# Kernel optimization log

Measured on AMD Instinct MI355X. Metric: run time of the kernel, lower is better.

## Reference

```python
import jax, jax.numpy as jnp
import numpy as np

T = 36  # num_frames


def box_cxcywh_to_xyxy(b):
    cx, cy, w, h = jnp.split(b, 4, axis=-1)
    return jnp.concatenate([cx - 0.5 * w, cy - 0.5 * h, cx + 0.5 * w, cy + 0.5 * h], axis=-1)


def multi_iou(b1, b2):
    # b1: [Q,1,T,4], b2: [1,N,T,4], xyxy -> iou [Q,N,T]
    lt = jnp.maximum(b1[..., :2], b2[..., :2])
    rb = jnp.minimum(b1[..., 2:], b2[..., 2:])
    wh = jnp.clip(rb - lt, 0.0)
    inter = wh[..., 0] * wh[..., 1]
    a1 = (b1[..., 2] - b1[..., 0]) * (b1[..., 3] - b1[..., 1])
    a2 = (b2[..., 2] - b2[..., 0]) * (b2[..., 3] - b2[..., 1])
    union = a1 + a2 - inter
    return inter / union


def setup_inputs() -> dict:
    key = jax.random.key(0)
    k1, k2, k3, k4, k5, k6 = jax.random.split(key, 6)
    Q, N, C = 2048, 128, 42
    return {
        "pred_logits": jax.random.normal(k1, (T * Q, C), dtype=jnp.float32),
        "pred_boxes": jax.random.uniform(k2, (T * Q, 4), dtype=jnp.float32),
        "tgt_labels": jax.random.randint(k3, (N * T,), 0, C - 1),
        "tgt_boxes": jax.random.uniform(k4, (N * T, 4), dtype=jnp.float32),
        "tgt_valid": jax.random.randint(k5, (N * T,), 0, 2, dtype=jnp.int32),
        "tgt_original_valid": jax.random.randint(k6, (N * T,), 0, 2, dtype=jnp.int32),
    }


def reference(pred_logits, pred_boxes, tgt_labels, tgt_boxes, tgt_valid, tgt_original_valid):
    # Cost-matrix computation of SoftMaxHungarianMatcher (cost_class=cost_bbox=cost_giou=1,
    # use_giou=False, use_l1_distance_sum=False). The scipy linear_sum_assignment step is
    # CPU-serial / non-tensor and excluded; output is the [Q,N] cost fed to it.
    C = pred_logits.shape[-1]
    Q = pred_logits.shape[0] // T
    N = tgt_labels.shape[0] // T
    num_classes = C - 1  # background index

    probs = jax.nn.softmax(pred_logits, axis=-1).reshape(T, Q, C).transpose(1, 0, 2)  # [Q,T,C]
    boxes = pred_boxes.reshape(T, Q, 4).transpose(1, 0, 2)                            # [Q,T,4]
    tboxes = tgt_boxes.reshape(N, T, 4)
    valid = tgt_valid.reshape(N, T).astype(probs.dtype)                               # [N,T]
    ovalid = tgt_original_valid.reshape(N, T)
    ids = jnp.where(ovalid == 0, num_classes, tgt_labels.reshape(N, T))               # [N,T]

    denom = valid.sum(-1)  # [N] (per-instance count of valid frames)

    # class cost: -mean_t p(q, t, ids[n,t]) over valid frames
    gathered = probs[:, jnp.arange(T)[None, :], ids]                                  # [Q,N,T]
    class_cost = -(gathered * valid).sum(-1) / denom                                  # [Q,N]

    # bbox L1 cost: mean over (valid frames, 4 coords)
    l1 = jnp.abs(boxes[:, None] - tboxes[None]).mean(-1)                              # [Q,N,T]
    bbox_cost = (l1 * valid).sum(-1) / denom                                          # [Q,N]

    # IoU cost: -mean_t iou over valid frames
    iou = multi_iou(box_cxcywh_to_xyxy(boxes)[:, None], box_cxcywh_to_xyxy(tboxes)[None])
    iou_cost = -(iou * valid).sum(-1) / denom                                         # [Q,N]

    return class_cost + bbox_cost + iou_cost
```

## Files before the change

kernel.cpp:

```cpp
#include <hip/hip_runtime.h>
#include <hip/hip_bf16.h>


constexpr int T = 36;
constexpr int Q = 2048;
constexpr int C = 42;
constexpr int N = 128;
constexpr int QB = 8;

__global__ __launch_bounds__(1024) void fused_kernel(
    const float* __restrict__ logits, const float* __restrict__ pboxes,
    const int* __restrict__ labels, const float* __restrict__ tboxes,
    const int* __restrict__ valid, const int* __restrict__ ovalid,
    float* __restrict__ out) {
  __shared__ float s_p[T * QB * C];
  __shared__ unsigned int s_idv[N * 9];
  __shared__ float s_out[QB * N];

  const int tid = threadIdx.x;
  const int q0 = blockIdx.x * QB;

  for (int i = tid; i < N * 9; i += 1024) {
    int n = i / 9;
    int t4 = (i - n * 9) * 4;
    unsigned int w = 0;
#pragma unroll
    for (int k = 0; k < 4; ++k) {
      int g = n * T + t4 + k;
      unsigned int id =
          (ovalid[g] == 0) ? (unsigned)(C - 1) : (unsigned)labels[g];
      w |= (id | (valid[g] ? 64u : 0u)) << (8 * k);
    }
    s_idv[i] = w;
  }

  for (int i = tid; i < T * 84; i += 1024) {
    int t = i / 84;
    int idx = i - t * 84;
    float4 v = ((const float4*)(logits + ((size_t)t * Q + q0) * C))[idx];
    float4 e;
    e.x = __expf(v.x);
    e.y = __expf(v.y);
    e.z = __expf(v.z);
    e.w = __expf(v.w);
    ((float4*)s_p)[t * 84 + idx] = e;
  }
  __syncthreads();

  if (tid < T * QB * 2) {
    const int r = tid >> 1;
    const int half = tid & 1;
    float* rowp = s_p + r * C + half * 21;
    float e[21];
    float s = 0.f;
#pragma unroll
    for (int k = 0; k < 21; ++k) {
      e[k] = rowp[k];
      s += e[k];
    }
    s += __shfl_xor(s, 1);
    float rs = __builtin_amdgcn_rcpf(s);
#pragma unroll
    for (int k = 0; k < 21; ++k) rowp[k] = e[k] * rs;
  }
  __syncthreads();

  const int qL = tid & 7;
  const int n = tid >> 3;
  const int q = q0 + qL;

  float acc = 0.f, sumv = 0.f;
  const unsigned int* idvp = s_idv + n * 9;
  const float* prow = s_p + qL * C;

  for (int tw = 0; tw < 9; ++tw) {
    unsigned int w = idvp[tw];
#pragma unroll
    for (int k = 0; k < 4; ++k) {
      const int t = tw * 4 + k;
      unsigned int b = (w >> (8 * k)) & 0xFFu;
      float vf = (float)(b >> 6);
      int id = (int)(b & 63u);
      float p = prow[(t * QB) * C + id];
      float4 pb = ((const float4*)pboxes)[t * Q + q];
      float4 tb = ((const float4*)tboxes)[n * T + t];

      float px1 = fmaf(-0.5f, pb.z, pb.x), py1 = fmaf(-0.5f, pb.w, pb.y);
      float px2 = fmaf(0.5f, pb.z, pb.x), py2 = fmaf(0.5f, pb.w, pb.y);
      float tx1 = fmaf(-0.5f, tb.z, tb.x), ty1 = fmaf(-0.5f, tb.w, tb.y);
      float tx2 = fmaf(0.5f, tb.z, tb.x), ty2 = fmaf(0.5f, tb.w, tb.y);

      float s4 = fabsf(pb.x - tb.x) + fabsf(pb.y - tb.y) +
                 fabsf(pb.z - tb.z) + fabsf(pb.w - tb.w);
      float iw = fmaxf(fminf(px2, tx2) - fmaxf(px1, tx1), 0.f);
      float ih = fmaxf(fminf(py2, ty2) - fmaxf(py1, ty1), 0.f);
      float inter = iw * ih;
      float uni = fmaf(tb.z, tb.w, pb.z * pb.w) - inter;
      float iou = inter * __builtin_amdgcn_rcpf(uni);
      float term = fmaf(0.25f, s4, -p) - iou;
      acc = fmaf(vf, term, acc);
      sumv += vf;
    }
  }

  s_out[qL * N + n] = acc * __builtin_amdgcn_rcpf(sumv);
  __syncthreads();

  if (tid < 256) {
    int qr = tid >> 5;
    int nf = tid & 31;
    float4 v = ((const float4*)s_out)[qr * 32 + nf];
    ((float4*)out)[(size_t)(q0 + qr) * (N / 4) + nf] = v;
  }
}

extern "C" void kernel_launch(void* const* d_in, const int* in_sizes, int n_in,
                              void* d_out, int out_size, void* d_ws, size_t ws_size,
                              hipStream_t stream) {
  const float* logits = (const float*)d_in[0];
  const float* pboxes = (const float*)d_in[1];
  const int* labels = (const int*)d_in[2];
  const float* tboxes = (const float*)d_in[3];
  const int* valid = (const int*)d_in[4];
  const int* ovalid = (const int*)d_in[5];
  float* out = (float*)d_out;

  fused_kernel<<<dim3(Q / QB), 1024, 0, stream>>>(logits, pboxes, labels,
                                                  tboxes, valid, ovalid, out);
}
```

Measured before the change: 84.55 us.

## Halve queries per block, split frames across thread halves, defer softmax normalization

New measurement: 84.65 us. Within noise of the previous version (+0.1%).

```diff
diff --git a/kernel.cpp b/kernel.cpp
--- a/kernel.cpp
+++ b/kernel.cpp
@@ -6,15 +6,18 @@
 constexpr int Q = 2048;
 constexpr int C = 42;
 constexpr int N = 128;
-constexpr int QB = 8;
+constexpr int QB = 4;
 
-__global__ __launch_bounds__(1024) void fused_kernel(
+__global__ __launch_bounds__(1024, 8) void fused_kernel(
     const float* __restrict__ logits, const float* __restrict__ pboxes,
     const int* __restrict__ labels, const float* __restrict__ tboxes,
     const int* __restrict__ valid, const int* __restrict__ ovalid,
     float* __restrict__ out) {
   __shared__ float s_p[T * QB * C];
   __shared__ unsigned int s_idv[N * 9];
+  __shared__ float s_rs[T * QB];
+  __shared__ float s_rden[N];
+  __shared__ float s_red[512];
   __shared__ float s_out[QB * N];
 
   const int tid = threadIdx.x;
@@ -34,56 +37,62 @@
     s_idv[i] = w;
   }
 
-  for (int i = tid; i < T * 84; i += 1024) {
-    int t = i / 84;
-    int idx = i - t * 84;
+  for (int i = tid; i < T * 42; i += 1024) {
+    int t = i / 42;
+    int idx = i - t * 42;
     float4 v = ((const float4*)(logits + ((size_t)t * Q + q0) * C))[idx];
     float4 e;
     e.x = __expf(v.x);
     e.y = __expf(v.y);
     e.z = __expf(v.z);
     e.w = __expf(v.w);
-    ((float4*)s_p)[t * 84 + idx] = e;
+    ((float4*)s_p)[i] = e;
   }
   __syncthreads();
 
   if (tid < T * QB * 2) {
     const int r = tid >> 1;
-    const int half = tid & 1;
-    float* rowp = s_p + r * C + half * 21;
-    float e[21];
+    const int hf = tid & 1;
+    const float* rowp = s_p + r * C + hf * 21;
     float s = 0.f;
 #pragma unroll
-    for (int k = 0; k < 21; ++k) {
-      e[k] = rowp[k];
-      s += e[k];
-    }
+    for (int k = 0; k < 21; ++k) s += rowp[k];
     s += __shfl_xor(s, 1);
-    float rs = __builtin_amdgcn_rcpf(s);
+    if (hf == 0) s_rs[r] = __builtin_amdgcn_rcpf(s);
+  } else if (tid >= 576 && tid < 576 + N) {
+    int n = tid - 576;
+    int cnt = 0;
 #pragma unroll
-    for (int k = 0; k < 21; ++k) rowp[k] = e[k] * rs;
+    for (int w9 = 0; w9 < 9; ++w9)
+      cnt += __popc(s_idv[n * 9 + w9] & 0x40404040u);
+    s_rden[n] = __builtin_amdgcn_rcpf((float)cnt);
   }
   __syncthreads();
 
-  const int qL = tid & 7;
-  const int n = tid >> 3;
+  const int qL = tid & 3;
+  const int n = (tid >> 2) & 127;
+  const int h = tid >> 9;
   const int q = q0 + qL;
 
-  float acc = 0.f, sumv = 0.f;
+  float acc = 0.f;
   const unsigned int* idvp = s_idv + n * 9;
+  const float4* pbq = (const float4*)pboxes + q;
+  const float4* tbn = (const float4*)tboxes + n * T;
   const float* prow = s_p + qL * C;
 
   for (int tw = 0; tw < 9; ++tw) {
     unsigned int w = idvp[tw];
 #pragma unroll
-    for (int k = 0; k < 4; ++k) {
+    for (int kk = 0; kk < 2; ++kk) {
+      const int k = h + 2 * kk;
       const int t = tw * 4 + k;
       unsigned int b = (w >> (8 * k)) & 0xFFu;
       float vf = (float)(b >> 6);
       int id = (int)(b & 63u);
-      float p = prow[(t * QB) * C + id];
-      float4 pb = ((const float4*)pboxes)[t * Q + q];
-      float4 tb = ((const float4*)tboxes)[n * T + t];
+      float e = prow[t * (QB * C) + id];
+      float p = e * s_rs[t * QB + qL];
+      float4 pb = pbq[(size_t)t * Q];
+      float4 tb = tbn[t];
 
       float px1 = fmaf(-0.5f, pb.z, pb.x), py1 = fmaf(-0.5f, pb.w, pb.y);
       float px2 = fmaf(0.5f, pb.z, pb.x), py2 = fmaf(0.5f, pb.w, pb.y);
@@ -99,14 +108,18 @@
       float iou = inter * __builtin_amdgcn_rcpf(uni);
       float term = fmaf(0.25f, s4, -p) - iou;
       acc = fmaf(vf, term, acc);
-      sumv += vf;
     }
   }
 
-  s_out[qL * N + n] = acc * __builtin_amdgcn_rcpf(sumv);
+  if (h == 1) s_red[tid - 512] = acc;
+  __syncthreads();
+  if (h == 0) {
+    float tot = (acc + s_red[tid]) * s_rden[n];
+    s_out[qL * N + n] = tot;
+  }
   __syncthreads();
 
-  if (tid < 256) {
+  if (tid < QB * N / 4) {
     int qr = tid >> 5;
     int nf = tid & 31;
     float4 v = ((const float4*)s_out)[qr * 32 + nf];
```
